# Kernel optimization log

Measured on AMD Instinct MI355X. Metric: run time of the kernel, lower is better.

Reference implementation:

```python
import jax, jax.numpy as jnp
import numpy as np

N = 10000      # n_nodes
FEAT = 512     # n_features
HID = 256
EMB = 128
NC = 10        # n_clusters
NE = 160000    # given edge count
K = 10         # topk for topology graph


def gcn_conv(x, W, b, src, dst, n):
    """PyG GCNConv: add self-loops, symmetric D^-1/2 (A+I) D^-1/2 X W + b."""
    h = x @ W  # [n, out]
    loop = jnp.arange(n)
    s = jnp.concatenate([src, loop])
    d = jnp.concatenate([dst, loop])
    deg = jax.ops.segment_sum(jnp.ones(s.shape[0], x.dtype), d, num_segments=n)
    dinv = jnp.where(deg > 0, deg ** -0.5, 0.0)
    norm = dinv[s] * dinv[d]  # [E+n]
    out = jax.ops.segment_sum(h[s] * norm[:, None], d, num_segments=n)
    return out + b


def setup_inputs() -> dict:
    key = jax.random.key(0)
    ks = jax.random.split(key, 8)
    return {
        "x": jax.random.normal(ks[0], (N, FEAT), jnp.float32),
        "edge_index": jax.random.randint(ks[1], (2, NE), 0, N),
        "W_s1": jax.random.normal(ks[2], (FEAT, HID), jnp.float32) * 0.05,
        "b_s1": jnp.zeros((HID,), jnp.float32),
        "W_s2": jax.random.normal(ks[3], (HID, EMB), jnp.float32) * 0.05,
        "b_s2": jnp.zeros((EMB,), jnp.float32),
        "W_t1": jax.random.normal(ks[4], (FEAT, HID), jnp.float32) * 0.05,
        "b_t1": jnp.zeros((HID,), jnp.float32),
        "W_t2": jax.random.normal(ks[5], (HID, EMB), jnp.float32) * 0.05,
        "b_t2": jnp.zeros((EMB,), jnp.float32),
        "fusion_weight": jnp.float32(0.5),
        "centroids": jax.random.normal(ks[6], (NC, EMB), jnp.float32),
    }


def reference(x, edge_index, W_s1, b_s1, W_s2, b_s2, W_t1, b_t1, W_t2, b_t2,
              fusion_weight, centroids):
    src, dst = edge_index[0], edge_index[1]
    # structural branch
    z_s = gcn_conv(x, W_s1, b_s1, src, dst, N)
    z_s = gcn_conv(jax.nn.relu(z_s), W_s2, b_s2, src, dst, N)
    # topology graph: cosine-sim kNN (vectorized replacement of python loop)
    x_norm = x / jnp.maximum(jnp.linalg.norm(x, axis=1, keepdims=True), 1e-12)
    sim = x_norm @ x_norm.T                       # [N, N]
    _, topk_idx = jax.lax.top_k(sim, K)           # [N, K]
    src_t = jnp.repeat(jnp.arange(N), K - 1)
    dst_t = topk_idx[:, 1:].reshape(-1)           # skip top-1 (self)
    # topology branch
    z_t = gcn_conv(x, W_t1, b_t1, src_t, dst_t, N)
    z_t = gcn_conv(jax.nn.relu(z_t), W_t2, b_t2, src_t, dst_t, N)
    # fusion
    beta = jax.nn.sigmoid(fusion_weight)
    z = beta * z_s + (1.0 - beta) * z_t           # [N, EMB]
    # soft cluster assignment (Student-t with dist^2)
    sq = jnp.sum((z[:, None, :] - centroids[None, :, :]) ** 2, axis=-1)  # [N, NC]
    q = 1.0 / (1.0 + sq)
    q = q / jnp.sum(q, axis=1, keepdims=True)
    return (z, q)
```

## Files before the change

### kernel.cpp

```cpp
#include <hip/hip_runtime.h>
#include <math.h>

#define N_NODES 10000
#define FEAT 512
#define HID 256
#define EMB 128
#define NC 10
#define NE_EDGES 160000
#define KTOP 10
#define NNB 9

#define CAP 128
#define NSEL 24
#define TAU 0.11f
#define SAFE_VAL 0.12f
#define NTB 79
#define NPAIR 3160
#define QCAP 2048

typedef __attribute__((ext_vector_type(8))) short short8;
typedef __attribute__((ext_vector_type(4))) float f32x4;

typedef const __attribute__((address_space(1))) unsigned int* gas1_t;
typedef __attribute__((address_space(3))) unsigned int* las3_t;

__device__ __forceinline__ void gload_lds16(const void* g, void* l) {
  __builtin_amdgcn_global_load_lds((gas1_t)g, (las3_t)l, 16, 0, 0);
}

__device__ __forceinline__ unsigned short f2h(float f) {
  _Float16 h = (_Float16)f;
  return *(unsigned short*)&h;
}
__device__ __forceinline__ float h2f(unsigned short u) {
  _Float16 h = *(_Float16*)&u;
  return (float)h;
}

__device__ __forceinline__ unsigned char f2e8(float f) {
  const unsigned u = __float_as_uint(f);
  const unsigned sg = (u >> 24) & 0x80u;
  const int e = (int)((u >> 23) & 0xffu) - 127;
  const unsigned m = u & 0x7fffffu;
  if (e >= -6) {
    if (e > 8) return sg | 0x7eu;
    unsigned mant = m >> 20;
    const unsigned rest = m & 0xfffffu;
    if (rest > 0x80000u || (rest == 0x80000u && (mant & 1u))) ++mant;
    unsigned ex = (unsigned)(e + 7);
    if (mant == 8u) { mant = 0u; ++ex; }
    if (ex > 15u || (ex == 15u && mant == 7u)) return sg | 0x7eu;
    return sg | (ex << 3) | mant;
  }
  const float af = fabsf(f);
  const int q = (int)(af * 512.0f + 0.5f);
  if (q > 7) return sg | 0x08u;
  return sg | (unsigned)q;
}

__global__ void k_norms(const float* __restrict__ x, unsigned char* __restrict__ xn8,
                        unsigned short* __restrict__ xf, double* __restrict__ rinv) {
  const int row = blockIdx.x;
  const int t = threadIdx.x;
  const float4 v = *(const float4*)(x + (size_t)row * FEAT + t * 4);
  double s = (double)v.x * v.x + (double)v.y * v.y + (double)v.z * v.z + (double)v.w * v.w;
  __shared__ double red[128];
  red[t] = s;
  __syncthreads();
  for (int o = 64; o > 0; o >>= 1) {
    if (t < o) red[t] += red[t + o];
    __syncthreads();
  }
  const double inv = 1.0 / fmax(sqrt(red[0]), 1e-12);
  const float finv = (float)inv;
  unsigned short hf[4] = {f2h(v.x), f2h(v.y), f2h(v.z), f2h(v.w)};
  *(uint2*)(xf + (size_t)row * FEAT + t * 4) = *(uint2*)hf;
  unsigned char e8[4] = {f2e8(v.x * finv), f2e8(v.y * finv), f2e8(v.z * finv),
                         f2e8(v.w * finv)};
  const int kb = t >> 4;
  const int ko = (t * 4) & 63;
  *(unsigned int*)(xn8 + ((size_t)kb * N_NODES + row) * 64 + ko) = *(unsigned int*)e8;
  if (t == 0) rinv[row] = inv;
}

__global__ void k_wtall(const float* __restrict__ W_s1, const float* __restrict__ W_t1,
                        const float* __restrict__ W_s2, const float* __restrict__ W_t2,
                        unsigned short* __restrict__ Wt_s1, unsigned short* __restrict__ Wt_t1,
                        unsigned short* __restrict__ Wt_s2, unsigned short* __restrict__ Wt_t2) {
  int idx = blockIdx.x * 256 + threadIdx.x;
  const int n1 = FEAT * HID;
  const int n2 = HID * EMB;
  if (idx < n1) {
    const int n = idx / FEAT, k = idx % FEAT;
    Wt_s1[idx] = f2h(W_s1[(size_t)k * HID + n]);
    return;
  }
  idx -= n1;
  if (idx < n1) {
    const int n = idx / FEAT, k = idx % FEAT;
    Wt_t1[idx] = f2h(W_t1[(size_t)k * HID + n]);
    return;
  }
  idx -= n1;
  if (idx < n2) {
    const int n = idx / HID, k = idx % HID;
    Wt_s2[idx] = f2h(W_s2[(size_t)k * EMB + n]);
    return;
  }
  idx -= n2;
  if (idx < n2) {
    const int n = idx / HID, k = idx % HID;
    Wt_t2[idx] = f2h(W_t2[(size_t)k * EMB + n]);
  }
}

__global__ __launch_bounds__(256) void k_simgemm(const unsigned char* __restrict__ xn8,
                                                 unsigned int* __restrict__ cap_buf,
                                                 int* __restrict__ cnt_row) {
  __shared__ __align__(16) unsigned char As[3][8192];
  __shared__ __align__(16) unsigned char Bs[3][8192];
  __shared__ int hn;

  const int t = threadIdx.x;
  const int lane = t & 63;
  const int w = t >> 6;
  const int lr = lane & 15;
  const int lk = lane >> 4;
  const int wr = (w >> 1) * 64, wc = (w & 1) * 64;

  const int bid = (blockIdx.x & 7) * 395 + (blockIdx.x >> 3);
  int bi = (int)((159.0 - sqrt(25281.0 - 8.0 * (double)bid)) * 0.5);
  while ((bi + 1) * NTB - (bi + 1) * bi / 2 <= bid) ++bi;
  while (bi * NTB - bi * (bi - 1) / 2 > bid) --bi;
  const int bj = bi + (bid - (bi * NTB - bi * (bi - 1) / 2));
  const int arow0 = bi * 128;
  const int bcol0 = bj * 128;

  auto stage = [&](int s, int k0) {
    const unsigned char* kbp = xn8 + (size_t)(k0 >> 6) * N_NODES * 64;
#pragma unroll
    for (int it = 0; it < 2; ++it) {
      const int slot = it * 256 + t;
      const int r = slot >> 2;
      const int qs = (slot & 3) ^ ((r >> 1) & 3);
      {
        const int gr = min(arow0 + r, N_NODES - 1);
        gload_lds16(kbp + (size_t)gr * 64 + qs * 16, &As[s][(it * 256 + w * 64) * 16]);
      }
      {
        const int gc = min(bcol0 + r, N_NODES - 1);
        gload_lds16(kbp + (size_t)gc * 64 + qs * 16, &Bs[s][(it * 256 + w * 64) * 16]);
      }
    }
  };

  f32x4 acc[4][4];
#pragma unroll
  for (int m = 0; m < 4; ++m)
#pragma unroll
    for (int n = 0; n < 4; ++n) acc[m][n] = (f32x4){0.f, 0.f, 0.f, 0.f};

  stage(0, 0);
  stage(1, 64);

  const int NT = FEAT / 64;
  int cur = 0, nxt = 2;
  for (int kt = 0; kt < NT; ++kt) {
    if (kt + 2 < NT) {
      stage(nxt, (kt + 2) * 64);
      asm volatile("s_waitcnt vmcnt(8)" ::: "memory");
    } else if (kt + 1 < NT) {
      asm volatile("s_waitcnt vmcnt(4)" ::: "memory");
    } else {
      asm volatile("s_waitcnt vmcnt(0)" ::: "memory");
    }
    __builtin_amdgcn_sched_barrier(0);
    __builtin_amdgcn_s_barrier();
    const unsigned char* Ab = As[cur];
    const unsigned char* Bb = Bs[cur];
    long av[2][4], bv[2][4];
#pragma unroll
    for (int h = 0; h < 2; ++h) {
#pragma unroll
      for (int m = 0; m < 4; ++m) {
        const int row = wr + m * 16 + lr;
        const int sl = (h * 2 + (lk >> 1)) ^ ((row >> 1) & 3);
        av[h][m] = *(const long*)(Ab + row * 64 + sl * 16 + (lk & 1) * 8);
      }
#pragma unroll
      for (int n = 0; n < 4; ++n) {
        const int row = wc + n * 16 + lr;
        const int sl = (h * 2 + (lk >> 1)) ^ ((row >> 1) & 3);
        bv[h][n] = *(const long*)(Bb + row * 64 + sl * 16 + (lk & 1) * 8);
      }
    }
    __builtin_amdgcn_s_setprio(1);
#pragma unroll
    for (int h = 0; h < 2; ++h)
#pragma unroll
      for (int m = 0; m < 4; ++m)
#pragma unroll
        for (int n = 0; n < 4; ++n)
          acc[m][n] =
              __builtin_amdgcn_mfma_f32_16x16x32_fp8_fp8(av[h][m], bv[h][n], acc[m][n], 0, 0, 0);
    __builtin_amdgcn_s_setprio(0);
    asm volatile("" ::: "memory");
    if (kt + 1 < NT) __builtin_amdgcn_s_barrier();
    cur = (cur == 2) ? 0 : cur + 1;
    nxt = (nxt == 2) ? 0 : nxt + 1;
  }

  __syncthreads();
  unsigned* hq = (unsigned*)&As[0][0];
  if (t == 0) hn = 0;
  __syncthreads();
  const bool offdiag = (bi != bj);
#pragma unroll
  for (int m = 0; m < 4; ++m) {
    const int lrow0 = wr + m * 16 + lk * 4;
#pragma unroll
    for (int n = 0; n < 4; ++n) {
      const int lcol = wc + n * 16 + lr;
#pragma unroll
      for (int q = 0; q < 4; ++q) {
        const float v = acc[m][n][q];
        if (v > TAU && (arow0 + lrow0 + q) < N_NODES && (bcol0 + lcol) < N_NODES) {
          const int p = atomicAdd(&hn, 1);
          if (p < QCAP)
            hq[p] = ((unsigned)f2h(v) << 16) | ((unsigned)(lrow0 + q) << 7) | (unsigned)lcol;
        }
      }
    }
  }
  __syncthreads();
  const int H = hn;
  if (H <= QCAP) {
    for (int e = t; e < H; e += 256) {
      const unsigned pk = hq[e];
      const int gr = arow0 + (int)((pk >> 7) & 127u);
      const int gc = bcol0 + (int)(pk & 127u);
      const unsigned hv = pk >> 16;
      {
        const int pos = atomicAdd(&cnt_row[gr], 1);
        if (pos < CAP) cap_buf[(size_t)gr * CAP + pos] = (hv << 16) | (unsigned)gc;
      }
      if (offdiag) {
        const int pos = atomicAdd(&cnt_row[gc], 1);
        if (pos < CAP) cap_buf[(size_t)gc * CAP + pos] = (hv << 16) | (unsigned)gr;
      }
    }
  } else {
#pragma unroll
    for (int m = 0; m < 4; ++m) {
      const int rb = arow0 + wr + m * 16 + lk * 4;
#pragma unroll
      for (int n = 0; n < 4; ++n) {
        const int gc = bcol0 + wc + n * 16 + lr;
        if (gc < N_NODES) {
#pragma unroll
          for (int q = 0; q < 4; ++q) {
            const float v = acc[m][n][q];
            const int gr = rb + q;
            if (v > TAU && gr < N_NODES) {
              const unsigned short hv = f2h(v);
              {
                const int pos = atomicAdd(&cnt_row[gr], 1);
                if (pos < CAP)
                  cap_buf[(size_t)gr * CAP + pos] = ((unsigned)hv << 16) | (unsigned)gc;
              }
              if (offdiag) {
                const int pos = atomicAdd(&cnt_row[gc], 1);
                if (pos < CAP)
                  cap_buf[(size_t)gc * CAP + pos] = ((unsigned)hv << 16) | (unsigned)gr;
              }
            }
          }
        }
      }
    }
  }
}

__global__ __launch_bounds__(256) void k_knn(const float* __restrict__ x,
                                             const double* __restrict__ rinv,
                                             const unsigned int* __restrict__ cap_buf,
                                             const int* __restrict__ cnt_row,
                                             int* __restrict__ nb, int* __restrict__ flags,
                                             int* __restrict__ cnt_t) {
  const int i = blockIdx.x;
  const int t = threadIdx.x;
  const int lane = t & 63;
  const int wave = t >> 6;
  __shared__ unsigned pp[CAP];
  __shared__ int sel[NSEL];
  __shared__ float xi[FEAT];
  __shared__ double dsv[NSEL];
  __shared__ int safe_cnt;

  const int cnt = cnt_row[i];
  if (cnt > CAP || cnt < NSEL) {
    if (t == 0) flags[i] = 1;
    return;
  }
  if (t == 0) { flags[i] = 0; safe_cnt = 0; }
  const int L = cnt;
  if (t < L) pp[t] = cap_buf[(size_t)i * CAP + t];
  xi[t] = x[(size_t)i * FEAT + t];
  xi[t + 256] = x[(size_t)i * FEAT + t + 256];
  __syncthreads();

  if (t < L) {
    const unsigned p = pp[t];
    if (h2f((unsigned short)(p >> 16)) >= SAFE_VAL) atomicAdd(&safe_cnt, 1);
    int rk = 0;
    for (int j = 0; j < L; ++j) rk += (pp[j] > p);
    if (rk < NSEL) sel[rk] = (int)(p & 0xffffu);
  }
  __syncthreads();
  if (safe_cnt < KTOP) {
    if (t == 0) flags[i] = 1;
    return;
  }

  const double ri = rinv[i];
  const float4 v0 = *(const float4*)(xi + lane * 8);
  const float4 v1 = *(const float4*)(xi + lane * 8 + 4);
#pragma unroll
  for (int q = 0; q < 6; ++q) {
    const int c = wave * 6 + q;
    const int ci = sel[c];
    const float4* xr = (const float4*)(x + (size_t)ci * FEAT);
    const float4 u0 = xr[lane * 2];
    const float4 u1 = xr[lane * 2 + 1];
    double s = (double)u0.x * (double)v0.x + (double)u0.y * (double)v0.y +
               (double)u0.z * (double)v0.z + (double)u0.w * (double)v0.w +
               (double)u1.x * (double)v1.x + (double)u1.y * (double)v1.y +
               (double)u1.z * (double)v1.z + (double)u1.w * (double)v1.w;
#pragma unroll
    for (int off = 1; off < 64; off <<= 1) s += __shfl_xor(s, off);
    if (lane == 0) dsv[c] = s * ri * rinv[ci];
  }
  __syncthreads();

  if (t < NSEL) {
    const double v = dsv[t];
    const int id = sel[t];
    int rk = 0;
    for (int j = 0; j < NSEL; ++j)
      rk += (dsv[j] > v) || (dsv[j] == v && sel[j] < id);
    if (rk >= 1 && rk < KTOP) {
      nb[(size_t)i * NNB + (rk - 1)] = id;
      atomicAdd(&cnt_t[id], 1);
    }
  }
}

__global__ __launch_bounds__(256) void k_fallback(const float* __restrict__ x,
                                                  const double* __restrict__ rinv,
                                                  const int* __restrict__ flags,
                                                  int* __restrict__ nb,
                                                  int* __restrict__ cnt_t) {
  const int i = blockIdx.x;
  if (!flags[i]) return;
  const int t = threadIdx.x;
  __shared__ float xi[FEAT];
  __shared__ double cval[256];
  __shared__ double bestv[NNB];
  __shared__ int besti[NNB];
  for (int k = t; k < FEAT; k += 256) xi[k] = x[(size_t)i * FEAT + k];
  if (t < NNB) { bestv[t] = -1e300; besti[t] = 0x7fffffff; }
  __syncthreads();
  const double ri = rinv[i];
  for (int c0 = 0; c0 < N_NODES; c0 += 256) {
    const int c = c0 + t;
    double s = -1e300;
    if (c < N_NODES && c != i) {
      s = 0.0;
      for (int k = 0; k < FEAT; ++k) s += (double)xi[k] * (double)x[(size_t)c * FEAT + k];
      s *= ri * rinv[c];
    }
    cval[t] = s;
    __syncthreads();
    if (t == 0) {
      for (int j = 0; j < 256; ++j) {
        const int c2 = c0 + j;
        const double v = cval[j];
        if (v == -1e300) continue;
        int pos = NNB;
        for (int q = 0; q < NNB; ++q) {
          if (v > bestv[q] || (v == bestv[q] && c2 < besti[q])) { pos = q; break; }
        }
        if (pos < NNB) {
          for (int q = NNB - 1; q > pos; --q) { bestv[q] = bestv[q - 1]; besti[q] = besti[q - 1]; }
          bestv[pos] = v; besti[pos] = c2;
        }
      }
    }
    __syncthreads();
  }
  if (t < NNB) {
    nb[(size_t)i * NNB + t] = besti[t];
    atomicAdd(&cnt_t[besti[t]], 1);
  }
}

__global__ void k_zero3(int* __restrict__ a, int* __restrict__ b, int* __restrict__ c) {
  const int i = blockIdx.x * blockDim.x + threadIdx.x;
  if (i < N_NODES) { a[i] = 0; b[i] = 0; c[i] = 0; }
}

__global__ void k_count(const int* __restrict__ dsts, int ne, int* __restrict__ cnt) {
  const int e = blockIdx.x * blockDim.x + threadIdx.x;
  if (e < ne) atomicAdd(&cnt[dsts[e]], 1);
}

__global__ void k_scan2(const int* __restrict__ cnt0, int* __restrict__ off0,
                        int* __restrict__ cur0, float* __restrict__ dinv0,
                        const int* __restrict__ cnt1, int* __restrict__ off1,
                        int* __restrict__ cur1, float* __restrict__ dinv1) {
  const int* cnt = blockIdx.x ? cnt1 : cnt0;
  int* off = blockIdx.x ? off1 : off0;
  int* cur = blockIdx.x ? cur1 : cur0;
  float* dinv = blockIdx.x ? dinv1 : dinv0;
  __shared__ int wsum[16];
  __shared__ int woff[16];
  __shared__ int base_s, tot_s;
  const int t = threadIdx.x;
  const int lane = t & 63, wid = t >> 6;
  if (t == 0) base_s = 0;
  __syncthreads();
  for (int b0 = 0; b0 < N_NODES; b0 += 1024) {
    const int i = b0 + t;
    const int v = (i < N_NODES) ? cnt[i] : 0;
    int inc = v;
#pragma unroll
    for (int o = 1; o < 64; o <<= 1) {
      const int u = __shfl_up(inc, o, 64);
      if (lane >= o) inc += u;
    }
    if (lane == 63) wsum[wid] = inc;
    __syncthreads();
    if (wid == 0) {
      const int ws = (lane < 16) ? wsum[lane] : 0;
      int wi = ws;
#pragma unroll
      for (int o = 1; o < 16; o <<= 1) {
        const int u = __shfl_up(wi, o, 64);
        if (lane >= o) wi += u;
      }
      if (lane < 16) woff[lane] = wi - ws;
      if (lane == 15) tot_s = wi;
    }
    __syncthreads();
    if (i < N_NODES) {
      const int excl = base_s + woff[wid] + (inc - v);
      off[i] = excl;
      cur[i] = excl;
      dinv[i] = rsqrtf((float)(v + 1));
    }
    __syncthreads();
    if (t == 0) base_s += tot_s;
    __syncthreads();
  }
  if (t == 0) off[N_NODES] = base_s;
}

__global__ void k_scatter_s(const int* __restrict__ src, const int* __restrict__ dst, int ne,
                            int* __restrict__ cur, int* __restrict__ csr) {
  const int e = blockIdx.x * blockDim.x + threadIdx.x;
  if (e < ne) {
    const int p = atomicAdd(&cur[dst[e]], 1);
    csr[p] = src[e];
  }
}

__global__ void k_scatter_t(const int* __restrict__ nb, int* __restrict__ cur,
                            int* __restrict__ csr) {
  const int e = blockIdx.x * blockDim.x + threadIdx.x;
  if (e < N_NODES * NNB) {
    const int i = e / NNB;
    const int v = nb[e];
    const int p = atomicAdd(&cur[v], 1);
    csr[p] = i;
  }
}

__global__ __launch_bounds__(256) void k_fgemm2(const unsigned short* __restrict__ A0,
                                                const unsigned short* __restrict__ A1,
                                                const unsigned short* __restrict__ Bt0,
                                                const unsigned short* __restrict__ Bt1,
                                                unsigned short* __restrict__ C0,
                                                unsigned short* __restrict__ C1,
                                                int M, int K, int N) {
  __shared__ __align__(16) unsigned short As[3][4096];
  __shared__ __align__(16) unsigned short Bs[3][4096];
  const int t = threadIdx.x;
  const int lane = t & 63, w = t >> 6;
  const int lr = lane & 15, lk = lane >> 4;
  const int wr = (w >> 1) * 64, wc = (w & 1) * 64;
  const int nbn = N >> 7;
  const int half = blockIdx.y / nbn;
  const unsigned short* A = half ? A1 : A0;
  const unsigned short* Bt = half ? Bt1 : Bt0;
  unsigned short* C = half ? C1 : C0;
  const int arow0 = blockIdx.x * 128, bcol0 = (blockIdx.y % nbn) * 128;

  auto stage = [&](int s, int k0) {
#pragma unroll
    for (int it = 0; it < 2; ++it) {
      const int slot = it * 256 + w * 64 + lane;
      const int r = slot >> 2;
      const int qs = (slot & 3) ^ ((r >> 1) & 3);
      {
        const int gr = min(arow0 + r, M - 1);
        gload_lds16(A + (size_t)gr * K + k0 + qs * 8, &As[s][(it * 256 + w * 64) * 8]);
      }
      {
        const int gc = min(bcol0 + r, N - 1);
        gload_lds16(Bt + (size_t)gc * K + k0 + qs * 8, &Bs[s][(it * 256 + w * 64) * 8]);
      }
    }
  };

  f32x4 acc[4][4];
#pragma unroll
  for (int m = 0; m < 4; ++m)
#pragma unroll
    for (int n = 0; n < 4; ++n) acc[m][n] = (f32x4){0.f, 0.f, 0.f, 0.f};

  stage(0, 0);
  if (K > 32) stage(1, 32);

  const int NT = K >> 5;
  int cur = 0, nxt = 2;
  for (int kt = 0; kt < NT; ++kt) {
    if (kt + 2 < NT) {
      stage(nxt, (kt + 2) << 5);
      asm volatile("s_waitcnt vmcnt(8)" ::: "memory");
    } else if (kt + 1 < NT) {
      asm volatile("s_waitcnt vmcnt(4)" ::: "memory");
    } else {
      asm volatile("s_waitcnt vmcnt(0)" ::: "memory");
    }
    __builtin_amdgcn_sched_barrier(0);
    __builtin_amdgcn_s_barrier();
    const unsigned short* Ab = As[cur];
    const unsigned short* Bb = Bs[cur];
    short8 a[4], b[4];
#pragma unroll
    for (int m = 0; m < 4; ++m) {
      const int row = wr + m * 16 + lr;
      a[m] = *(const short8*)(Ab + (((row << 2) | (lk ^ ((row >> 1) & 3))) << 3));
    }
#pragma unroll
    for (int n = 0; n < 4; ++n) {
      const int row = wc + n * 16 + lr;
      b[n] = *(const short8*)(Bb + (((row << 2) | (lk ^ ((row >> 1) & 3))) << 3));
    }
    __builtin_amdgcn_s_setprio(1);
#pragma unroll
    for (int m = 0; m < 4; ++m)
#pragma unroll
      for (int n = 0; n < 4; ++n)
        acc[m][n] = __builtin_amdgcn_mfma_f32_16x16x32_f16(a[m], b[n], acc[m][n], 0, 0, 0);
    __builtin_amdgcn_s_setprio(0);
    asm volatile("" ::: "memory");
    if (kt + 1 < NT) __builtin_amdgcn_s_barrier();
    cur = (cur == 2) ? 0 : cur + 1;
    nxt = (nxt == 2) ? 0 : nxt + 1;
  }

#pragma unroll
  for (int m = 0; m < 4; ++m) {
    const int rb = arow0 + wr + m * 16 + lk * 4;
#pragma unroll
    for (int n = 0; n < 4; ++n) {
      const int gc = bcol0 + wc + n * 16 + lr;
#pragma unroll
      for (int q = 0; q < 4; ++q) {
        const int gm = rb + q;
        if (gm < M) C[(size_t)gm * N + gc] = f2h(acc[m][n][q]);
      }
    }
  }
}

__global__ void k_agg_h2(const unsigned short* __restrict__ h0,
                         const unsigned short* __restrict__ h1,
                         const float* __restrict__ bias0, const float* __restrict__ bias1,
                         const float* __restrict__ dinv0, const float* __restrict__ dinv1,
                         const int* __restrict__ off0, const int* __restrict__ off1,
                         const int* __restrict__ csr0, const int* __restrict__ csr1,
                         unsigned short* __restrict__ out0, unsigned short* __restrict__ out1) {
  const int br = blockIdx.y;
  const unsigned short* h = br ? h1 : h0;
  const float* bias = br ? bias1 : bias0;
  const float* dinv = br ? dinv1 : dinv0;
  const int* off = br ? off1 : off0;
  const int* csr = br ? csr1 : csr0;
  unsigned short* out = br ? out1 : out0;
  const int v = blockIdx.x;
  const int c = threadIdx.x;
  const float dv = dinv[v];
  float acc = h2f(h[(size_t)v * HID + c]) * dv;
  const int s0 = off[v], s1 = off[v + 1];
  int e = s0;
  for (; e + 1 < s1; e += 2) {
    const int sa = csr[e], sb = csr[e + 1];
    const float ha = h2f(h[(size_t)sa * HID + c]), hb = h2f(h[(size_t)sb * HID + c]);
    acc += ha * dinv[sa] + hb * dinv[sb];
  }
  if (e < s1) {
    const int sa = csr[e];
    acc += h2f(h[(size_t)sa * HID + c]) * dinv[sa];
  }
  acc = acc * dv + bias[c];
  out[(size_t)v * HID + c] = f2h(fmaxf(acc, 0.f));
}

__global__ void k_aggfuse(const unsigned short* __restrict__ h2_s,
                          const unsigned short* __restrict__ h2_t,
                          const float* __restrict__ b_s2, const float* __restrict__ b_t2,
                          const float* __restrict__ dinv_s, const int* __restrict__ off_s,
                          const int* __restrict__ csr_s, const float* __restrict__ dinv_t,
                          const int* __restrict__ off_t, const int* __restrict__ csr_t,
                          const float* __restrict__ fw, const float* __restrict__ cent,
                          float* __restrict__ out_z, float* __restrict__ out_q) {
  const int v = blockIdx.x;
  const int c = threadIdx.x;
  __shared__ float zsh[EMB];
  __shared__ float cs[NC][EMB];
  __shared__ float qv[NC];
  __shared__ float qs;
  for (int k = c; k < NC * EMB; k += 128) ((float*)cs)[k] = cent[k];
  float zs, zt;
  {
    const float dv = dinv_s[v];
    float acc = h2f(h2_s[(size_t)v * EMB + c]) * dv;
    const int s0 = off_s[v], s1 = off_s[v + 1];
    int e = s0;
    for (; e + 1 < s1; e += 2) {
      const int sa = csr_s[e], sb = csr_s[e + 1];
      acc += h2f(h2_s[(size_t)sa * EMB + c]) * dinv_s[sa] +
             h2f(h2_s[(size_t)sb * EMB + c]) * dinv_s[sb];
    }
    if (e < s1) {
      const int sa = csr_s[e];
      acc += h2f(h2_s[(size_t)sa * EMB + c]) * dinv_s[sa];
    }
    zs = acc * dv + b_s2[c];
  }
  {
    const float dv = dinv_t[v];
    float acc = h2f(h2_t[(size_t)v * EMB + c]) * dv;
    const int s0 = off_t[v], s1 = off_t[v + 1];
    int e = s0;
    for (; e + 1 < s1; e += 2) {
      const int sa = csr_t[e], sb = csr_t[e + 1];
      acc += h2f(h2_t[(size_t)sa * EMB + c]) * dinv_t[sa] +
             h2f(h2_t[(size_t)sb * EMB + c]) * dinv_t[sb];
    }
    if (e < s1) {
      const int sa = csr_t[e];
      acc += h2f(h2_t[(size_t)sa * EMB + c]) * dinv_t[sa];
    }
    zt = acc * dv + b_t2[c];
  }
  const float beta = 1.f / (1.f + expf(-fw[0]));
  const float z = beta * zs + (1.f - beta) * zt;
  out_z[(size_t)v * EMB + c] = z;
  zsh[c] = z;
  __syncthreads();
  if (c < NC) {
    float s = 0.f;
    for (int k = 0; k < EMB; ++k) {
      const float d = zsh[k] - cs[c][k];
      s += d * d;
    }
    qv[c] = 1.f / (1.f + s);
  }
  __syncthreads();
  if (c == 0) {
    float s = 0.f;
    for (int k = 0; k < NC; ++k) s += qv[k];
    qs = s;
  }
  __syncthreads();
  if (c < NC) out_q[(size_t)v * NC + c] = qv[c] / qs;
}

extern "C" void kernel_launch(void* const* d_in, const int* in_sizes, int n_in, void* d_out,
                              int out_size, void* d_ws, size_t ws_size, hipStream_t stream) {
  const float* x = (const float*)d_in[0];
  const int* ei = (const int*)d_in[1];
  const float* W_s1 = (const float*)d_in[2];
  const float* b_s1 = (const float*)d_in[3];
  const float* W_s2 = (const float*)d_in[4];
  const float* b_s2 = (const float*)d_in[5];
  const float* W_t1 = (const float*)d_in[6];
  const float* b_t1 = (const float*)d_in[7];
  const float* W_t2 = (const float*)d_in[8];
  const float* b_t2 = (const float*)d_in[9];
  const float* fw = (const float*)d_in[10];
  const float* cent = (const float*)d_in[11];
  float* out_z = (float*)d_out;
  float* out_q = out_z + (size_t)N_NODES * EMB;

  char* w = (char*)d_ws;
  size_t o = 0;
  auto alloc = [&](size_t bytes) -> void* {
    void* p = w + o;
    o += (bytes + 255) & ~(size_t)255;
    return p;
  };
  unsigned char* xn8 = (unsigned char*)alloc((size_t)N_NODES * FEAT * 2);
  unsigned short* h1_s = (unsigned short*)xn8;
  unsigned short* xf = (unsigned short*)alloc((size_t)N_NODES * FEAT * 2);
  unsigned short* h2_s = xf;
  unsigned short* h2_t = xf + (size_t)N_NODES * EMB;
  double* rinv = (double*)alloc((size_t)N_NODES * 8);
  unsigned int* cap_buf = (unsigned int*)alloc((size_t)N_NODES * CAP * 4);
  unsigned short* r1_s = (unsigned short*)cap_buf;
  unsigned short* r1_t = (unsigned short*)alloc((size_t)N_NODES * HID * 2);
  unsigned short* h1_t = (unsigned short*)alloc((size_t)N_NODES * HID * 2);
  int* nb = (int*)alloc((size_t)N_NODES * NNB * 4);
  int* cnt_s = (int*)alloc((size_t)N_NODES * 4);
  int* off_s = (int*)alloc((size_t)(N_NODES + 1) * 4);
  int* cur_s = (int*)alloc((size_t)N_NODES * 4);
  float* dinv_s = (float*)alloc((size_t)N_NODES * 4);
  int* cnt_t = (int*)alloc((size_t)N_NODES * 4);
  int* off_t = (int*)alloc((size_t)(N_NODES + 1) * 4);
  int* cur_t = (int*)alloc((size_t)N_NODES * 4);
  float* dinv_t = (float*)alloc((size_t)N_NODES * 4);
  int* csr_s = (int*)alloc((size_t)NE_EDGES * 4);
  int* csr_t = (int*)alloc((size_t)N_NODES * NNB * 4);
  int* cnt_row = (int*)alloc((size_t)N_NODES * 4);
  int* flags = (int*)alloc((size_t)N_NODES * 4);
  unsigned short* Wt_s1 = (unsigned short*)alloc((size_t)FEAT * HID * 2);
  unsigned short* Wt_t1 = (unsigned short*)alloc((size_t)FEAT * HID * 2);
  unsigned short* Wt_s2 = (unsigned short*)alloc((size_t)HID * EMB * 2);
  unsigned short* Wt_t2 = (unsigned short*)alloc((size_t)HID * EMB * 2);

  const int* e_src = ei;
  const int* e_dst = ei + NE_EDGES;

  k_norms<<<N_NODES, 128, 0, stream>>>(x, xn8, xf, rinv);
  {
    const int tot = 2 * FEAT * HID + 2 * HID * EMB;
    k_wtall<<<(tot + 255) / 256, 256, 0, stream>>>(W_s1, W_t1, W_s2, W_t2, Wt_s1, Wt_t1, Wt_s2,
                                                   Wt_t2);
  }
  k_zero3<<<(N_NODES + 255) / 256, 256, 0, stream>>>(cnt_s, cnt_t, cnt_row);
  k_count<<<(NE_EDGES + 255) / 256, 256, 0, stream>>>(e_dst, NE_EDGES, cnt_s);
  k_simgemm<<<NPAIR, 256, 0, stream>>>(xn8, cap_buf, cnt_row);
  k_knn<<<N_NODES, 256, 0, stream>>>(x, rinv, cap_buf, cnt_row, nb, flags, cnt_t);
  k_fallback<<<N_NODES, 256, 0, stream>>>(x, rinv, flags, nb, cnt_t);
  k_scan2<<<2, 1024, 0, stream>>>(cnt_s, off_s, cur_s, dinv_s, cnt_t, off_t, cur_t, dinv_t);
  k_scatter_s<<<(NE_EDGES + 255) / 256, 256, 0, stream>>>(e_src, e_dst, NE_EDGES, cur_s, csr_s);
  k_scatter_t<<<(N_NODES * NNB + 255) / 256, 256, 0, stream>>>(nb, cur_t, csr_t);
  {
    dim3 g1(NTB, 2 * (HID / 128));
    k_fgemm2<<<g1, 256, 0, stream>>>(xf, xf, Wt_s1, Wt_t1, h1_s, h1_t, N_NODES, FEAT, HID);
  }
  {
    dim3 ga(N_NODES, 2);
    k_agg_h2<<<ga, HID, 0, stream>>>(h1_s, h1_t, b_s1, b_t1, dinv_s, dinv_t, off_s, off_t, csr_s,
                                     csr_t, r1_s, r1_t);
  }
  {
    dim3 g2(NTB, 2 * (EMB / 128));
    k_fgemm2<<<g2, 256, 0, stream>>>(r1_s, r1_t, Wt_s2, Wt_t2, h2_s, h2_t, N_NODES, HID, EMB);
  }
  k_aggfuse<<<N_NODES, EMB, 0, stream>>>(h2_s, h2_t, b_s2, b_t2, dinv_s, off_s, csr_s, dinv_t,
                                         off_t, csr_t, fw, cent, out_z, out_q);
}
```

Measured before the change: 333.5 us.

## Enlarge similarity GEMM tiles to 256x256 with 512-thread blocks

The symmetric cosine-similarity FP8 GEMM now uses 256x256 output tiles over the upper triangle (820 blocks of 512 threads) instead of 128x128 tiles (3160 blocks of 256 threads). Each wave holds 8x4 accumulators, and LDS staging buffers are doubled. The goal is more operand reuse per byte loaded and fewer blocks, at the cost of more registers, 96KB of LDS per block, and lower occupancy. The kNN refinement kernel also processes two candidate dot products per iteration so their loads and shuffle reductions can overlap.

```diff
diff --git a/kernel.cpp b/kernel.cpp
--- a/kernel.cpp
+++ b/kernel.cpp
@@ -15,8 +15,9 @@
 #define TAU 0.11f
 #define SAFE_VAL 0.12f
 #define NTB 79
-#define NPAIR 3160
-#define QCAP 2048
+#define NTB2 40
+#define NPAIR2 820
+#define QCAP2 8192
 
 typedef __attribute__((ext_vector_type(8))) short short8;
 typedef __attribute__((ext_vector_type(4))) float f32x4;
@@ -114,49 +115,50 @@
   }
 }
 
-__global__ __launch_bounds__(256) void k_simgemm(const unsigned char* __restrict__ xn8,
+__global__ __launch_bounds__(512) void k_simgemm(const unsigned char* __restrict__ xn8,
                                                  unsigned int* __restrict__ cap_buf,
                                                  int* __restrict__ cnt_row) {
-  __shared__ __align__(16) unsigned char As[3][8192];
-  __shared__ __align__(16) unsigned char Bs[3][8192];
-  __shared__ int hn;
+  __shared__ __align__(16) unsigned char As[3][16384];
+  __shared__ __align__(16) unsigned char Bs[3][16384];
 
   const int t = threadIdx.x;
   const int lane = t & 63;
   const int w = t >> 6;
   const int lr = lane & 15;
   const int lk = lane >> 4;
-  const int wr = (w >> 1) * 64, wc = (w & 1) * 64;
-
-  const int bid = (blockIdx.x & 7) * 395 + (blockIdx.x >> 3);
-  int bi = (int)((159.0 - sqrt(25281.0 - 8.0 * (double)bid)) * 0.5);
-  while ((bi + 1) * NTB - (bi + 1) * bi / 2 <= bid) ++bi;
-  while (bi * NTB - bi * (bi - 1) / 2 > bid) --bi;
-  const int bj = bi + (bid - (bi * NTB - bi * (bi - 1) / 2));
-  const int arow0 = bi * 128;
-  const int bcol0 = bj * 128;
+  const int wr = (w >> 2) * 128;
+  const int wc = (w & 3) * 64;
+
+  const int xcd = blockIdx.x & 7;
+  const int idx = blockIdx.x >> 3;
+  const int wg = (xcd < 4) ? xcd * 103 + idx : 4 * 103 + (xcd - 4) * 102 + idx;
+  int bi = 0;
+  while ((bi + 1) * NTB2 - (bi + 1) * bi / 2 <= wg) ++bi;
+  const int bj = bi + (wg - (bi * NTB2 - bi * (bi - 1) / 2));
+  const int arow0 = bi * 256;
+  const int bcol0 = bj * 256;
 
   auto stage = [&](int s, int k0) {
     const unsigned char* kbp = xn8 + (size_t)(k0 >> 6) * N_NODES * 64;
 #pragma unroll
     for (int it = 0; it < 2; ++it) {
-      const int slot = it * 256 + t;
+      const int slot = it * 512 + t;
       const int r = slot >> 2;
       const int qs = (slot & 3) ^ ((r >> 1) & 3);
       {
         const int gr = min(arow0 + r, N_NODES - 1);
-        gload_lds16(kbp + (size_t)gr * 64 + qs * 16, &As[s][(it * 256 + w * 64) * 16]);
+        gload_lds16(kbp + (size_t)gr * 64 + qs * 16, &As[s][(it * 512 + w * 64) * 16]);
       }
       {
         const int gc = min(bcol0 + r, N_NODES - 1);
-        gload_lds16(kbp + (size_t)gc * 64 + qs * 16, &Bs[s][(it * 256 + w * 64) * 16]);
+        gload_lds16(kbp + (size_t)gc * 64 + qs * 16, &Bs[s][(it * 512 + w * 64) * 16]);
       }
     }
   };
 
-  f32x4 acc[4][4];
-#pragma unroll
-  for (int m = 0; m < 4; ++m)
+  f32x4 acc[8][4];
+#pragma unroll
+  for (int m = 0; m < 8; ++m)
 #pragma unroll
     for (int n = 0; n < 4; ++n) acc[m][n] = (f32x4){0.f, 0.f, 0.f, 0.f};
 
@@ -178,32 +180,29 @@
     __builtin_amdgcn_s_barrier();
     const unsigned char* Ab = As[cur];
     const unsigned char* Bb = Bs[cur];
-    long av[2][4], bv[2][4];
 #pragma unroll
     for (int h = 0; h < 2; ++h) {
-#pragma unroll
-      for (int m = 0; m < 4; ++m) {
+      long av[8], bv[4];
+#pragma unroll
+      for (int m = 0; m < 8; ++m) {
         const int row = wr + m * 16 + lr;
         const int sl = (h * 2 + (lk >> 1)) ^ ((row >> 1) & 3);
-        av[h][m] = *(const long*)(Ab + row * 64 + sl * 16 + (lk & 1) * 8);
+        av[m] = *(const long*)(Ab + row * 64 + sl * 16 + (lk & 1) * 8);
       }
 #pragma unroll
       for (int n = 0; n < 4; ++n) {
         const int row = wc + n * 16 + lr;
         const int sl = (h * 2 + (lk >> 1)) ^ ((row >> 1) & 3);
-        bv[h][n] = *(const long*)(Bb + row * 64 + sl * 16 + (lk & 1) * 8);
-      }
-    }
-    __builtin_amdgcn_s_setprio(1);
-#pragma unroll
-    for (int h = 0; h < 2; ++h)
-#pragma unroll
-      for (int m = 0; m < 4; ++m)
+        bv[n] = *(const long*)(Bb + row * 64 + sl * 16 + (lk & 1) * 8);
+      }
+      __builtin_amdgcn_s_setprio(1);
+#pragma unroll
+      for (int m = 0; m < 8; ++m)
 #pragma unroll
         for (int n = 0; n < 4; ++n)
-          acc[m][n] =
-              __builtin_amdgcn_mfma_f32_16x16x32_fp8_fp8(av[h][m], bv[h][n], acc[m][n], 0, 0, 0);
-    __builtin_amdgcn_s_setprio(0);
+          acc[m][n] = __builtin_amdgcn_mfma_f32_16x16x32_fp8_fp8(av[m], bv[n], acc[m][n], 0, 0, 0);
+      __builtin_amdgcn_s_setprio(0);
+    }
     asm volatile("" ::: "memory");
     if (kt + 1 < NT) __builtin_amdgcn_s_barrier();
     cur = (cur == 2) ? 0 : cur + 1;
@@ -212,11 +211,12 @@
 
   __syncthreads();
   unsigned* hq = (unsigned*)&As[0][0];
-  if (t == 0) hn = 0;
+  int* hnp = (int*)&Bs[0][0];
+  if (t == 0) *hnp = 0;
   __syncthreads();
   const bool offdiag = (bi != bj);
 #pragma unroll
-  for (int m = 0; m < 4; ++m) {
+  for (int m = 0; m < 8; ++m) {
     const int lrow0 = wr + m * 16 + lk * 4;
 #pragma unroll
     for (int n = 0; n < 4; ++n) {
@@ -225,20 +225,20 @@
       for (int q = 0; q < 4; ++q) {
         const float v = acc[m][n][q];
         if (v > TAU && (arow0 + lrow0 + q) < N_NODES && (bcol0 + lcol) < N_NODES) {
-          const int p = atomicAdd(&hn, 1);
-          if (p < QCAP)
-            hq[p] = ((unsigned)f2h(v) << 16) | ((unsigned)(lrow0 + q) << 7) | (unsigned)lcol;
+          const int p = atomicAdd(hnp, 1);
+          if (p < QCAP2)
+            hq[p] = ((unsigned)f2h(v) << 16) | ((unsigned)(lrow0 + q) << 8) | (unsigned)lcol;
         }
       }
     }
   }
   __syncthreads();
-  const int H = hn;
-  if (H <= QCAP) {
-    for (int e = t; e < H; e += 256) {
+  const int H = *hnp;
+  if (H <= QCAP2) {
+    for (int e = t; e < H; e += 512) {
       const unsigned pk = hq[e];
-      const int gr = arow0 + (int)((pk >> 7) & 127u);
-      const int gc = bcol0 + (int)(pk & 127u);
+      const int gr = arow0 + (int)((pk >> 8) & 255u);
+      const int gc = bcol0 + (int)(pk & 255u);
       const unsigned hv = pk >> 16;
       {
         const int pos = atomicAdd(&cnt_row[gr], 1);
@@ -251,7 +251,7 @@
     }
   } else {
 #pragma unroll
-    for (int m = 0; m < 4; ++m) {
+    for (int m = 0; m < 8; ++m) {
       const int rb = arow0 + wr + m * 16 + lk * 4;
 #pragma unroll
       for (int n = 0; n < 4; ++n) {
@@ -326,19 +326,32 @@
   const float4 v0 = *(const float4*)(xi + lane * 8);
   const float4 v1 = *(const float4*)(xi + lane * 8 + 4);
 #pragma unroll
-  for (int q = 0; q < 6; ++q) {
-    const int c = wave * 6 + q;
-    const int ci = sel[c];
-    const float4* xr = (const float4*)(x + (size_t)ci * FEAT);
-    const float4 u0 = xr[lane * 2];
-    const float4 u1 = xr[lane * 2 + 1];
-    double s = (double)u0.x * (double)v0.x + (double)u0.y * (double)v0.y +
-               (double)u0.z * (double)v0.z + (double)u0.w * (double)v0.w +
-               (double)u1.x * (double)v1.x + (double)u1.y * (double)v1.y +
-               (double)u1.z * (double)v1.z + (double)u1.w * (double)v1.w;
-#pragma unroll
-    for (int off = 1; off < 64; off <<= 1) s += __shfl_xor(s, off);
-    if (lane == 0) dsv[c] = s * ri * rinv[ci];
+  for (int qq = 0; qq < 6; qq += 2) {
+    const int c0i = wave * 6 + qq, c1i = c0i + 1;
+    const int ci0 = sel[c0i], ci1 = sel[c1i];
+    const float4* xr0 = (const float4*)(x + (size_t)ci0 * FEAT);
+    const float4* xr1 = (const float4*)(x + (size_t)ci1 * FEAT);
+    const float4 a0 = xr0[lane * 2];
+    const float4 a1 = xr0[lane * 2 + 1];
+    const float4 b0 = xr1[lane * 2];
+    const float4 b1 = xr1[lane * 2 + 1];
+    double s0 = (double)a0.x * (double)v0.x + (double)a0.y * (double)v0.y +
+                (double)a0.z * (double)v0.z + (double)a0.w * (double)v0.w +
+                (double)a1.x * (double)v1.x + (double)a1.y * (double)v1.y +
+                (double)a1.z * (double)v1.z + (double)a1.w * (double)v1.w;
+    double s1 = (double)b0.x * (double)v0.x + (double)b0.y * (double)v0.y +
+                (double)b0.z * (double)v0.z + (double)b0.w * (double)v0.w +
+                (double)b1.x * (double)v1.x + (double)b1.y * (double)v1.y +
+                (double)b1.z * (double)v1.z + (double)b1.w * (double)v1.w;
+#pragma unroll
+    for (int off = 1; off < 64; off <<= 1) {
+      s0 += __shfl_xor(s0, off);
+      s1 += __shfl_xor(s1, off);
+    }
+    if (lane == 0) {
+      dsv[c0i] = s0 * ri * rinv[ci0];
+      dsv[c1i] = s1 * ri * rinv[ci1];
+    }
   }
   __syncthreads();
 
@@ -752,7 +765,7 @@
   }
   k_zero3<<<(N_NODES + 255) / 256, 256, 0, stream>>>(cnt_s, cnt_t, cnt_row);
   k_count<<<(NE_EDGES + 255) / 256, 256, 0, stream>>>(e_dst, NE_EDGES, cnt_s);
-  k_simgemm<<<NPAIR, 256, 0, stream>>>(xn8, cap_buf, cnt_row);
+  k_simgemm<<<NPAIR2, 512, 0, stream>>>(xn8, cap_buf, cnt_row);
   k_knn<<<N_NODES, 256, 0, stream>>>(x, rinv, cap_buf, cnt_row, nb, flags, cnt_t);
   k_fallback<<<N_NODES, 256, 0, stream>>>(x, rinv, flags, nb, cnt_t);
   k_scan2<<<2, 1024, 0, stream>>>(cnt_s, off_s, cur_s, dinv_s, cnt_t, off_t, cur_t, dinv_t);
```

After: 335.1 us. About the same (+0.5%).
